# Kernel optimization log

Hardware: AMD Instinct MI355X
Metric: run time of the kernel (lower is better)

The kernel has to match this reference:

```python
import jax, jax.numpy as jnp
import numpy as np

N, C, H, W = 2, 256, 128, 128
NH, P = 8, 4
DH = C // NH
PAD = 1            # int(sqrt(n_points)//2)
HP, WP = H + 2 * PAD, W + 2 * PAD
LQ = H * W
DW_KS = 7


def _grid():
    # _generate_dilation_grids with n_points=4, dilation_rates=[1]:
    # kernel_size=2, linspace(0,1,2); torch stacks [y, x] (y-first quirk preserved)
    lin = np.linspace(0.0, 1.0, 2, dtype=np.float32)
    ky, kx = np.meshgrid(lin, lin, indexing='ij')
    return jnp.asarray(np.stack([ky, kx], -1).reshape(P, 2))  # (P, 2)


def _forward(query, reference_points, dw_kernel, dw_bias, ln_w, ln_b,
             W_off, b_off, W_attn, b_attn, W_val, b_val, W_out, b_out):
    # ---- dw_conv branch: depthwise 7x7 conv + channel LayerNorm + exact GELU ----
    q_img = query.transpose(0, 2, 1).reshape(N, C, H, W)
    q_img = jax.lax.conv_general_dilated(
        q_img, dw_kernel, (1, 1), [(3, 3), (3, 3)],
        dimension_numbers=('NCHW', 'OIHW', 'NCHW'), feature_group_count=C
    ) + dw_bias[None, :, None, None]
    mu = q_img.mean(axis=1, keepdims=True)
    var = ((q_img - mu) ** 2).mean(axis=1, keepdims=True)
    q_img = (q_img - mu) * jax.lax.rsqrt(var + 1e-5) * ln_w[None, :, None, None] + ln_b[None, :, None, None]
    q_img = jax.nn.gelu(q_img, approximate=False)
    q = q_img.transpose(0, 2, 3, 1).reshape(N, LQ, C)

    # ---- value projection + zero padding around the H x W map ----
    value = q @ W_val + b_val
    value = jnp.pad(value.reshape(N, H, W, C), ((0, 0), (PAD, PAD), (PAD, PAD), (0, 0)))
    v = value.reshape(N, HP * WP, NH, DH).transpose(0, 2, 1, 3)  # (N, NH, S, DH)

    # ---- offsets, sigmoid attention weights ----
    off = (q @ W_off + b_off).reshape(N, LQ, NH, 1, P, 2)
    attn = jax.nn.sigmoid(q @ W_attn + b_attn).reshape(N, LQ, NH, P)  # n_levels=1

    grid = _grid()[None, None, None, None, :, :]               # (1,1,1,1,P,2)
    norm = jnp.array([WP, HP], dtype=query.dtype)              # (W, H) normalizer
    loc = reference_points[:, :, None, :, None, :] + (grid + off) / norm
    loc = loc[:, :, :, 0, :, :]                                # (N, LQ, NH, P, 2)

    # grid_sample bilinear, align_corners=False, zero padding
    x = loc[..., 0] * WP - 0.5
    y = loc[..., 1] * HP - 0.5
    x0 = jnp.floor(x)
    y0 = jnp.floor(y)
    wx1 = x - x0
    wx0 = 1.0 - wx1
    wy1 = y - y0
    wy0 = 1.0 - wy1
    x0i = x0.astype(jnp.int32)
    y0i = y0.astype(jnp.int32)

    def gather(xi, yi):
        valid = (xi >= 0) & (xi < WP) & (yi >= 0) & (yi < HP)
        idx = jnp.clip(yi, 0, HP - 1) * WP + jnp.clip(xi, 0, WP - 1)
        idx = idx.transpose(0, 2, 1, 3).reshape(N, NH, LQ * P)
        g = jnp.take_along_axis(v, idx[..., None], axis=2)     # (N, NH, LQ*P, DH)
        m = valid.transpose(0, 2, 1, 3).reshape(N, NH, LQ * P, 1)
        return jnp.where(m, g, 0.0)

    def wmul(w):
        return w.transpose(0, 2, 1, 3).reshape(N, NH, LQ * P, 1)

    samp = (gather(x0i, y0i) * wmul(wx0 * wy0)
            + gather(x0i + 1, y0i) * wmul(wx1 * wy0)
            + gather(x0i, y0i + 1) * wmul(wx0 * wy1)
            + gather(x0i + 1, y0i + 1) * wmul(wx1 * wy1))      # (N, NH, LQ*P, DH)

    samp = samp.reshape(N, NH, LQ, P, DH)
    aw = attn.transpose(0, 2, 1, 3)[..., None]                 # (N, NH, LQ, P, 1)
    out = (samp * aw).sum(axis=3)                              # (N, NH, LQ, DH)
    out = out.transpose(0, 2, 1, 3).reshape(N, LQ, C)
    return out @ W_out + b_out


def setup_inputs() -> dict:
    key = jax.random.key(0)
    ks = jax.random.split(key, 8)
    return dict(
        query=jax.random.normal(ks[0], (N, LQ, C), jnp.float32),
        reference_points=jax.random.uniform(ks[1], (N, LQ, 1, 2), dtype=jnp.float32),
        input_spatial_shapes=jnp.array([[HP, WP]], dtype=jnp.int32),
        input_level_start_index=jnp.zeros((1,), dtype=jnp.int32),
        dw_kernel=jax.random.normal(ks[2], (C, 1, DW_KS, DW_KS), jnp.float32) * 0.05,
        dw_bias=jnp.zeros((C,), jnp.float32),
        ln_w=jnp.ones((C,), jnp.float32),
        ln_b=jnp.zeros((C,), jnp.float32),
        W_off=jax.random.normal(ks[3], (C, NH * P * 2), jnp.float32) * 0.01,
        b_off=jnp.zeros((NH * P * 2,), jnp.float32),
        W_attn=jax.random.normal(ks[4], (C, NH * P), jnp.float32) * 0.02,
        b_attn=jnp.zeros((NH * P,), jnp.float32),
        W_val=jax.random.normal(ks[5], (C, C), jnp.float32) * (1.0 / 16.0),
        b_val=jnp.zeros((C,), jnp.float32),
        W_out=jax.random.normal(ks[6], (C, C), jnp.float32) * (1.0 / 16.0),
        b_out=jnp.zeros((C,), jnp.float32),
    )


def reference(query, reference_points, input_spatial_shapes, input_level_start_index,
              dw_kernel, dw_bias, ln_w, ln_b, W_off, b_off, W_attn, b_attn,
              W_val, b_val, W_out, b_out):
    # input_spatial_shapes / input_level_start_index are static metadata (baked into constants)
    return _forward(query, reference_points, dw_kernel, dw_bias, ln_w, ln_b,
                    W_off, b_off, W_attn, b_attn, W_val, b_val, W_out, b_out)
```

## Files before the change

kernel.cpp:

```cpp
#include <hip/hip_runtime.h>
#include <hip/hip_bf16.h>
#include <math.h>

#define NB   2
#define CC   256
#define HH   128
#define WW   128
#define HPP  130
#define WPP  130
#define LQ   16384

typedef __attribute__((ext_vector_type(8))) short short8;
typedef __attribute__((ext_vector_type(4))) float f32x4;
typedef __attribute__((ext_vector_type(4))) unsigned int u32x4;

static __device__ __forceinline__ unsigned short f2bf(float f) {
    __hip_bfloat16 h = __float2bfloat16(f);
    return __builtin_bit_cast(unsigned short, h);
}
static __device__ __forceinline__ float bf2f(unsigned short u) {
    unsigned int x = ((unsigned int)u) << 16;
    return __builtin_bit_cast(float, x);
}

static __device__ __forceinline__ float gelu_fast(float x) {
    float u = x * x;
    float t = x * fmaf(0.044715f, u, 1.0f);
    float e = __builtin_amdgcn_exp2f(t * 2.3022083f);
    float r = __builtin_amdgcn_rcpf(e + 1.0f);
    return x - x * r;
}

__global__ __launch_bounds__(256) void prep_kernel(
    const float* __restrict__ dwk,
    const float* __restrict__ Wval,
    const float* __restrict__ Wout,
    const float* __restrict__ Woff, const float* __restrict__ boff,
    const float* __restrict__ Wattn, const float* __restrict__ battn,
    float* __restrict__ kt,
    unsigned short* __restrict__ wt_val,
    unsigned short* __restrict__ wt_out,
    unsigned short* __restrict__ wt_oa,
    float* __restrict__ b_oa)
{
    int b = blockIdx.x;
    int t = threadIdx.x;
    if (b < 49) {
        kt[b * CC + t] = dwk[t * 49 + b];
    } else if (b < 305) {
        int k = b - 49;
        wt_val[(size_t)t * 256 + k] = f2bf(Wval[(size_t)k * 256 + t]);
    } else if (b < 561) {
        int k = b - 305;
        wt_out[(size_t)t * 256 + k] = f2bf(Wout[(size_t)k * 256 + t]);
    } else {
        int k = b - 561;
        if (t < 128) {
            float v = 0.f, bb = 0.f;
            if (t < 64)      { v = Woff[(size_t)k * 64 + t];        bb = boff[t]; }
            else if (t < 96) { v = Wattn[(size_t)k * 32 + (t - 64)]; bb = battn[t - 64]; }
            wt_oa[(size_t)t * 256 + k] = f2bf(v);
            if (k == 0) b_oa[t] = bb;
        }
    }
}

__global__ __launch_bounds__(256) void zero_border_kernel(unsigned short* __restrict__ vpad)
{
    int b = blockIdx.x;
    int n = (b >= 516) ? 1 : 0;
    int i = b - n * 516;
    int y, x;
    if (i < 130)      { y = 0;           x = i; }
    else if (i < 260) { y = 129;         x = i - 130; }
    else if (i < 388) { y = i - 260 + 1; x = 0; }
    else              { y = i - 388 + 1; x = 129; }
    vpad[(((size_t)n * HPP + y) * WPP + x) * CC + threadIdx.x] = 0;
}

__global__ __launch_bounds__(256) void conv_ln_gelu_kernel(
    const float* __restrict__ q,
    const float* __restrict__ kt,
    const float* __restrict__ kbias,
    const float* __restrict__ lnw,
    const float* __restrict__ lnb,
    unsigned short* __restrict__ qact)
{
    int c  = threadIdx.x;
    int w0 = blockIdx.x * 8;
    int h  = blockIdx.y;
    int n  = blockIdx.z;

    const float* qn = q + (size_t)n * LQ * CC + c;

    float bias = kbias[c];
    float acc[8];
    #pragma unroll
    for (int i = 0; i < 8; ++i) acc[i] = bias;

    if (w0 >= 8 && w0 <= 112 && h >= 3 && h <= 124) {
        #pragma unroll
        for (int ky = 0; ky < 7; ++ky) {
            const float* qrow = qn + ((size_t)(h + ky - 3) * WW + (w0 - 3)) * CC;
            float wt[7];
            #pragma unroll
            for (int kx = 0; kx < 7; ++kx)
                wt[kx] = kt[(ky * 7 + kx) * CC + c];
            float in[14];
            #pragma unroll
            for (int j = 0; j < 14; ++j)
                in[j] = qrow[(size_t)j * CC];
            #pragma unroll
            for (int i = 0; i < 8; ++i)
                #pragma unroll
                for (int kx = 0; kx < 7; ++kx)
                    acc[i] = fmaf(in[i + kx], wt[kx], acc[i]);
        }
    } else {
        #pragma unroll
        for (int ky = 0; ky < 7; ++ky) {
            int iy = h + ky - 3;
            if (iy < 0 || iy >= HH) continue;
            float wt[7];
            #pragma unroll
            for (int kx = 0; kx < 7; ++kx)
                wt[kx] = kt[(ky * 7 + kx) * CC + c];
            float in[14];
            const float* qrow = qn + (size_t)iy * WW * CC;
            #pragma unroll
            for (int j = 0; j < 14; ++j) {
                int ix = w0 - 3 + j;
                in[j] = (ix >= 0 && ix < WW) ? qrow[(size_t)ix * CC] : 0.f;
            }
            #pragma unroll
            for (int i = 0; i < 8; ++i)
                #pragma unroll
                for (int kx = 0; kx < 7; ++kx)
                    acc[i] = fmaf(in[i + kx], wt[kx], acc[i]);
        }
    }

    __shared__ float lsum[8][4];
    __shared__ float lsq[8][4];
    int lane = threadIdx.x & 63;
    int wv   = threadIdx.x >> 6;

    #pragma unroll
    for (int i = 0; i < 8; ++i) {
        float v  = acc[i];
        float v2 = v * v;
        #pragma unroll
        for (int m = 1; m < 64; m <<= 1) {
            v  += __shfl_xor(v,  m);
            v2 += __shfl_xor(v2, m);
        }
        if (lane == 0) { lsum[i][wv] = v; lsq[i][wv] = v2; }
    }
    __syncthreads();

    float lw = lnw[c];
    float lb = lnb[c];
    unsigned short* qo = qact + (((size_t)n * LQ) + (size_t)h * WW + w0) * CC + c;

    #pragma unroll
    for (int i = 0; i < 8; ++i) {
        float s  = lsum[i][0] + lsum[i][1] + lsum[i][2] + lsum[i][3];
        float s2 = lsq[i][0]  + lsq[i][1]  + lsq[i][2]  + lsq[i][3];
        float mu  = s * (1.0f / 256.0f);
        float var = s2 * (1.0f / 256.0f) - mu * mu;
        float inv = rsqrtf(var + 1e-5f);
        float yv  = (acc[i] - mu) * inv * lw + lb;
        qo[(size_t)i * CC] = f2bf(gelu_fast(yv));
    }
}

__global__ __launch_bounds__(256) void gemm_val_oa(
    const unsigned short* __restrict__ A,
    const unsigned short* __restrict__ Bv, const float* __restrict__ bv_,
    unsigned short* __restrict__ Cv,
    const unsigned short* __restrict__ Bo, const float* __restrict__ bo_,
    float* __restrict__ Co)
{
    __shared__ unsigned short Al[128][72];
    __shared__ unsigned short Bl[128][72];

    bool oam = (blockIdx.y == 2);
    const unsigned short* Bt = oam ? Bo : Bv;
    const float* bias = oam ? bo_ : bv_;
    int bn = oam ? 0 : blockIdx.y * 128;

    int t    = threadIdx.x;
    int bm   = blockIdx.x * 128;
    int wid  = t >> 6;
    int lane = t & 63;
    int wr   = wid >> 1;
    int wc   = wid & 1;
    int lr   = lane & 15;
    int lg   = lane >> 4;

    int srow = t >> 1;
    int sseg = (t & 1) << 5;

    const unsigned short* gA = A + (size_t)(bm + srow) * 256 + sseg;
    const unsigned short* gB = Bt + (size_t)(bn + srow) * 256 + sseg;
    unsigned short* lA = &Al[srow][sseg];
    unsigned short* lB = &Bl[srow][sseg];

    f32x4 acc[4][4] = {};

    for (int kt = 0; kt < 4; ++kt) {
        const unsigned short* ga = gA + kt * 64;
        const unsigned short* gb = gB + kt * 64;
        u32x4 a0 = *(const u32x4*)(ga);
        u32x4 a1 = *(const u32x4*)(ga + 8);
        u32x4 a2 = *(const u32x4*)(ga + 16);
        u32x4 a3 = *(const u32x4*)(ga + 24);
        u32x4 b0 = *(const u32x4*)(gb);
        u32x4 b1 = *(const u32x4*)(gb + 8);
        u32x4 b2 = *(const u32x4*)(gb + 16);
        u32x4 b3 = *(const u32x4*)(gb + 24);
        *(u32x4*)(lA)      = a0;
        *(u32x4*)(lA + 8)  = a1;
        *(u32x4*)(lA + 16) = a2;
        *(u32x4*)(lA + 24) = a3;
        *(u32x4*)(lB)      = b0;
        *(u32x4*)(lB + 8)  = b1;
        *(u32x4*)(lB + 16) = b2;
        *(u32x4*)(lB + 24) = b3;
        __syncthreads();

        #pragma unroll
        for (int kk = 0; kk < 2; ++kk) {
            short8 af[4], bfr[4];
            #pragma unroll
            for (int m = 0; m < 4; ++m)
                af[m] = *(const short8*)(&Al[wr * 64 + m * 16 + lr][kk * 32 + lg * 8]);
            #pragma unroll
            for (int nn = 0; nn < 4; ++nn)
                bfr[nn] = *(const short8*)(&Bl[wc * 64 + nn * 16 + lr][kk * 32 + lg * 8]);
            #pragma unroll
            for (int m = 0; m < 4; ++m)
                #pragma unroll
                for (int nn = 0; nn < 4; ++nn)
                    acc[m][nn] = __builtin_amdgcn_mfma_f32_16x16x32_bf16(
                        af[m], bfr[nn], acc[m][nn], 0, 0, 0);
        }
        __syncthreads();
    }

    float bvv[4];
    #pragma unroll
    for (int nn = 0; nn < 4; ++nn) bvv[nn] = bias[bn + wc * 64 + nn * 16 + lr];

    #pragma unroll
    for (int m = 0; m < 4; ++m) {
        #pragma unroll
        for (int j = 0; j < 4; ++j) {
            int row = bm + wr * 64 + m * 16 + lg * 4 + j;
            if (oam) {
                size_t rbase = (size_t)row * 128;
                #pragma unroll
                for (int nn = 0; nn < 4; ++nn) {
                    int col = wc * 64 + nn * 16 + lr;
                    Co[rbase + col] = acc[m][nn][j] + bvv[nn];
                }
            } else {
                int nb = row >> 14;
                int hw = row & 16383;
                int hh = hw >> 7;
                int ww = hw & 127;
                size_t rbase = (((size_t)nb * HPP + (hh + 1)) * WPP + (ww + 1)) * CC;
                #pragma unroll
                for (int nn = 0; nn < 4; ++nn) {
                    int col = bn + wc * 64 + nn * 16 + lr;
                    Cv[rbase + col] = f2bf(acc[m][nn][j] + bvv[nn]);
                }
            }
        }
    }
}

__global__ __launch_bounds__(256) void gemm_mfma_row(
    const unsigned short* __restrict__ A,
    const unsigned short* __restrict__ Bt,
    const float* __restrict__ bias,
    float* __restrict__ C,
    int Nn)
{
    __shared__ unsigned short Al[128][72];
    __shared__ unsigned short Bl[128][72];

    int t    = threadIdx.x;
    int bm   = blockIdx.x * 128;
    int bn   = blockIdx.y * 128;
    int wid  = t >> 6;
    int lane = t & 63;
    int wr   = wid >> 1;
    int wc   = wid & 1;
    int lr   = lane & 15;
    int lg   = lane >> 4;

    int srow = t >> 1;
    int sseg = (t & 1) << 5;

    const unsigned short* gA = A + (size_t)(bm + srow) * 256 + sseg;
    const unsigned short* gB = Bt + (size_t)(bn + srow) * 256 + sseg;
    unsigned short* lA = &Al[srow][sseg];
    unsigned short* lB = &Bl[srow][sseg];

    f32x4 acc[4][4] = {};

    for (int kt = 0; kt < 4; ++kt) {
        const unsigned short* ga = gA + kt * 64;
        const unsigned short* gb = gB + kt * 64;
        u32x4 a0 = *(const u32x4*)(ga);
        u32x4 a1 = *(const u32x4*)(ga + 8);
        u32x4 a2 = *(const u32x4*)(ga + 16);
        u32x4 a3 = *(const u32x4*)(ga + 24);
        u32x4 b0 = *(const u32x4*)(gb);
        u32x4 b1 = *(const u32x4*)(gb + 8);
        u32x4 b2 = *(const u32x4*)(gb + 16);
        u32x4 b3 = *(const u32x4*)(gb + 24);
        *(u32x4*)(lA)      = a0;
        *(u32x4*)(lA + 8)  = a1;
        *(u32x4*)(lA + 16) = a2;
        *(u32x4*)(lA + 24) = a3;
        *(u32x4*)(lB)      = b0;
        *(u32x4*)(lB + 8)  = b1;
        *(u32x4*)(lB + 16) = b2;
        *(u32x4*)(lB + 24) = b3;
        __syncthreads();

        #pragma unroll
        for (int kk = 0; kk < 2; ++kk) {
            short8 af[4], bfr[4];
            #pragma unroll
            for (int m = 0; m < 4; ++m)
                af[m] = *(const short8*)(&Al[wr * 64 + m * 16 + lr][kk * 32 + lg * 8]);
            #pragma unroll
            for (int nn = 0; nn < 4; ++nn)
                bfr[nn] = *(const short8*)(&Bl[wc * 64 + nn * 16 + lr][kk * 32 + lg * 8]);
            #pragma unroll
            for (int m = 0; m < 4; ++m)
                #pragma unroll
                for (int nn = 0; nn < 4; ++nn)
                    acc[m][nn] = __builtin_amdgcn_mfma_f32_16x16x32_bf16(
                        af[m], bfr[nn], acc[m][nn], 0, 0, 0);
        }
        __syncthreads();
    }

    float bvv[4];
    #pragma unroll
    for (int nn = 0; nn < 4; ++nn) bvv[nn] = bias[bn + wc * 64 + nn * 16 + lr];

    #pragma unroll
    for (int m = 0; m < 4; ++m) {
        #pragma unroll
        for (int j = 0; j < 4; ++j) {
            int row = bm + wr * 64 + m * 16 + lg * 4 + j;
            size_t rbase = (size_t)row * Nn;
            #pragma unroll
            for (int nn = 0; nn < 4; ++nn) {
                int col = bn + wc * 64 + nn * 16 + lr;
                C[rbase + col] = acc[m][nn][j] + bvv[nn];
            }
        }
    }
}

__global__ __launch_bounds__(256) void sampler_kernel(
    const float* __restrict__ rp,
    const float* __restrict__ oa,
    const unsigned short* __restrict__ vpad,
    unsigned short* __restrict__ outb)
{
    __shared__ int4   sIdx[4][4][8];
    __shared__ float4 sW[4][4][8];

    int tid  = threadIdx.x;
    int row0 = blockIdx.x * 4;

    if (tid < 128) {
        int rl   = tid >> 5;
        int hp   = tid & 31;
        int head = hp >> 2;
        int p    = hp & 3;
        int row  = row0 + rl;

        float ref0 = rp[(size_t)row * 2 + 0];
        float ref1 = rp[(size_t)row * 2 + 1];
        float o0 = oa[(size_t)row * 128 + head * 8 + p * 2 + 0];
        float o1 = oa[(size_t)row * 128 + head * 8 + p * 2 + 1];
        float al = oa[(size_t)row * 128 + 64 + head * 4 + p];
        float a  = 1.0f / (1.0f + __builtin_amdgcn_exp2f(-al * 1.4426950409f));

        float gy = (float)(p >> 1);
        float gx = (float)(p & 1);
        float x = ref0 * WPP + gy + o0 - 0.5f;
        float y = ref1 * HPP + gx + o1 - 0.5f;

        float x0f = floorf(x), y0f = floorf(y);
        int   x0  = (int)x0f,  y0  = (int)y0f;
        float wx1 = x - x0f, wx0 = 1.f - wx1;
        float wy1 = y - y0f, wy0 = 1.f - wy1;
        int x1 = x0 + 1, y1 = y0 + 1;

        bool vx0 = (x0 >= 0) & (x0 < WPP);
        bool vx1 = (x1 >= 0) & (x1 < WPP);
        bool vy0 = (y0 >= 0) & (y0 < HPP);
        bool vy1 = (y1 >= 0) & (y1 < HPP);
        int cx0 = min(max(x0, 0), WPP - 1);
        int cx1 = min(max(x1, 0), WPP - 1);
        int cy0 = min(max(y0, 0), HPP - 1);
        int cy1 = min(max(y1, 0), HPP - 1);

        int4 id;
        id.x = cy0 * WPP + cx0;
        id.y = cy0 * WPP + cx1;
        id.z = cy1 * WPP + cx0;
        id.w = cy1 * WPP + cx1;
        float4 w;
        w.x = (vx0 && vy0) ? a * wx0 * wy0 : 0.f;
        w.y = (vx1 && vy0) ? a * wx1 * wy0 : 0.f;
        w.z = (vx0 && vy1) ? a * wx0 * wy1 : 0.f;
        w.w = (vx1 && vy1) ? a * wx1 * wy1 : 0.f;

        sIdx[rl][p][head] = id;
        sW[rl][p][head]   = w;
    }
    __syncthreads();

    int rl   = tid >> 6;
    int c0   = (tid & 63) * 4;
    int head = c0 >> 5;
    int row  = row0 + rl;
    int n    = row >> 14;
    const unsigned short* vbase = vpad + (size_t)n * HPP * WPP * CC + c0;

    float4 acc = make_float4(0.f, 0.f, 0.f, 0.f);
    #pragma unroll
    for (int p = 0; p < 4; ++p) {
        int4   id = sIdx[rl][p][head];
        float4 w  = sW[rl][p][head];
        ushort4 g0 = *reinterpret_cast<const ushort4*>(vbase + (size_t)id.x * CC);
        ushort4 g1 = *reinterpret_cast<const ushort4*>(vbase + (size_t)id.y * CC);
        ushort4 g2 = *reinterpret_cast<const ushort4*>(vbase + (size_t)id.z * CC);
        ushort4 g3 = *reinterpret_cast<const ushort4*>(vbase + (size_t)id.w * CC);
        acc.x += w.x * bf2f(g0.x) + w.y * bf2f(g1.x) + w.z * bf2f(g2.x) + w.w * bf2f(g3.x);
        acc.y += w.x * bf2f(g0.y) + w.y * bf2f(g1.y) + w.z * bf2f(g2.y) + w.w * bf2f(g3.y);
        acc.z += w.x * bf2f(g0.z) + w.y * bf2f(g1.z) + w.z * bf2f(g2.z) + w.w * bf2f(g3.z);
        acc.w += w.x * bf2f(g0.w) + w.y * bf2f(g1.w) + w.z * bf2f(g2.w) + w.w * bf2f(g3.w);
    }
    ushort4 o;
    o.x = f2bf(acc.x);
    o.y = f2bf(acc.y);
    o.z = f2bf(acc.z);
    o.w = f2bf(acc.w);
    *reinterpret_cast<ushort4*>(&outb[(size_t)row * CC + c0]) = o;
}

extern "C" void kernel_launch(void* const* d_in, const int* in_sizes, int n_in,
                              void* d_out, int out_size, void* d_ws, size_t ws_size,
                              hipStream_t stream)
{
    const float* query = (const float*)d_in[0];
    const float* rp    = (const float*)d_in[1];
    const float* dwk   = (const float*)d_in[4];
    const float* dwb   = (const float*)d_in[5];
    const float* lnw   = (const float*)d_in[6];
    const float* lnb   = (const float*)d_in[7];
    const float* Woff  = (const float*)d_in[8];
    const float* boff  = (const float*)d_in[9];
    const float* Wattn = (const float*)d_in[10];
    const float* battn = (const float*)d_in[11];
    const float* Wval  = (const float*)d_in[12];
    const float* bval  = (const float*)d_in[13];
    const float* Wout  = (const float*)d_in[14];
    const float* bout  = (const float*)d_in[15];
    float* out = (float*)d_out;

    const int M = NB * LQ;

    uint8_t* w8 = (uint8_t*)d_ws;
    unsigned short* q_act  = (unsigned short*)w8;
    unsigned short* v_pad  = (unsigned short*)(w8 + 16777216);
    float*          oa     = (float*)(w8 + 34082816);
    unsigned short* wt_val = (unsigned short*)(w8 + 50860032);
    unsigned short* wt_out = (unsigned short*)(w8 + 50991104);
    unsigned short* wt_oa  = (unsigned short*)(w8 + 51122176);
    float*          b_oa   = (float*)(w8 + 51187712);
    float*          kt     = (float*)(w8 + 51188224);
    unsigned short* out_attn = q_act;

    zero_border_kernel<<<1032, 256, 0, stream>>>(v_pad);

    prep_kernel<<<817, 256, 0, stream>>>(
        dwk, Wval, Wout, Woff, boff, Wattn, battn,
        kt, wt_val, wt_out, wt_oa, b_oa);

    {
        dim3 grid(WW / 8, HH, NB);
        conv_ln_gelu_kernel<<<grid, 256, 0, stream>>>(
            query, kt, dwb, lnw, lnb, q_act);
    }

    {
        dim3 grid(M / 128, 3);
        gemm_val_oa<<<grid, 256, 0, stream>>>(
            q_act, wt_val, bval, v_pad, wt_oa, b_oa, oa);
    }

    sampler_kernel<<<M / 4, 256, 0, stream>>>(rp, oa, v_pad, out_attn);

    {
        dim3 grid(M / 128, 2);
        gemm_mfma_row<<<grid, 256, 0, stream>>>(out_attn, wt_out, bout, out, 256);
    }
}
```

Before: 96.59 us.

## Compute two output rows per conv block and fold border zeroing into prep kernel

```diff
diff --git a/kernel.cpp b/kernel.cpp
--- a/kernel.cpp
+++ b/kernel.cpp
@@ -41,7 +41,8 @@
     unsigned short* __restrict__ wt_val,
     unsigned short* __restrict__ wt_out,
     unsigned short* __restrict__ wt_oa,
-    float* __restrict__ b_oa)
+    float* __restrict__ b_oa,
+    unsigned short* __restrict__ vpad)
 {
     int b = blockIdx.x;
     int t = threadIdx.x;
@@ -53,7 +54,7 @@
     } else if (b < 561) {
         int k = b - 305;
         wt_out[(size_t)t * 256 + k] = f2bf(Wout[(size_t)k * 256 + t]);
-    } else {
+    } else if (b < 817) {
         int k = b - 561;
         if (t < 128) {
             float v = 0.f, bb = 0.f;
@@ -62,20 +63,17 @@
             wt_oa[(size_t)t * 256 + k] = f2bf(v);
             if (k == 0) b_oa[t] = bb;
         }
-    }
-}
-
-__global__ __launch_bounds__(256) void zero_border_kernel(unsigned short* __restrict__ vpad)
-{
-    int b = blockIdx.x;
-    int n = (b >= 516) ? 1 : 0;
-    int i = b - n * 516;
-    int y, x;
-    if (i < 130)      { y = 0;           x = i; }
-    else if (i < 260) { y = 129;         x = i - 130; }
-    else if (i < 388) { y = i - 260 + 1; x = 0; }
-    else              { y = i - 388 + 1; x = 129; }
-    vpad[(((size_t)n * HPP + y) * WPP + x) * CC + threadIdx.x] = 0;
+    } else {
+        int bb = b - 817;
+        int n = (bb >= 516) ? 1 : 0;
+        int i = bb - n * 516;
+        int y, x;
+        if (i < 130)      { y = 0;           x = i; }
+        else if (i < 260) { y = 129;         x = i - 130; }
+        else if (i < 388) { y = i - 260 + 1; x = 0; }
+        else              { y = i - 388 + 1; x = 129; }
+        vpad[(((size_t)n * HPP + y) * WPP + x) * CC + t] = 0;
+    }
 }
 
 __global__ __launch_bounds__(256) void conv_ln_gelu_kernel(
@@ -88,66 +86,95 @@
 {
     int c  = threadIdx.x;
     int w0 = blockIdx.x * 8;
-    int h  = blockIdx.y;
+    int h0 = blockIdx.y * 2;
     int n  = blockIdx.z;
 
     const float* qn = q + (size_t)n * LQ * CC + c;
+    const float* ktc = kt + c;
 
     float bias = kbias[c];
-    float acc[8];
-    #pragma unroll
-    for (int i = 0; i < 8; ++i) acc[i] = bias;
-
-    if (w0 >= 8 && w0 <= 112 && h >= 3 && h <= 124) {
-        #pragma unroll
-        for (int ky = 0; ky < 7; ++ky) {
-            const float* qrow = qn + ((size_t)(h + ky - 3) * WW + (w0 - 3)) * CC;
-            float wt[7];
-            #pragma unroll
-            for (int kx = 0; kx < 7; ++kx)
-                wt[kx] = kt[(ky * 7 + kx) * CC + c];
+    float acc0[8], acc1[8];
+    #pragma unroll
+    for (int i = 0; i < 8; ++i) { acc0[i] = bias; acc1[i] = bias; }
+
+    float wt_prev[7];
+
+    if (w0 >= 8 && w0 <= 112 && h0 >= 3 && h0 <= 123) {
+        #pragma unroll
+        for (int r = 0; r < 8; ++r) {
+            const float* qrow = qn + ((size_t)(h0 - 3 + r) * WW + (w0 - 3)) * CC;
             float in[14];
             #pragma unroll
             for (int j = 0; j < 14; ++j)
                 in[j] = qrow[(size_t)j * CC];
-            #pragma unroll
-            for (int i = 0; i < 8; ++i)
+            float wt_cur[7];
+            if (r < 7) {
                 #pragma unroll
                 for (int kx = 0; kx < 7; ++kx)
-                    acc[i] = fmaf(in[i + kx], wt[kx], acc[i]);
+                    wt_cur[kx] = ktc[(r * 7 + kx) * CC];
+                #pragma unroll
+                for (int i = 0; i < 8; ++i)
+                    #pragma unroll
+                    for (int kx = 0; kx < 7; ++kx)
+                        acc0[i] = fmaf(in[i + kx], wt_cur[kx], acc0[i]);
+            }
+            if (r >= 1) {
+                #pragma unroll
+                for (int i = 0; i < 8; ++i)
+                    #pragma unroll
+                    for (int kx = 0; kx < 7; ++kx)
+                        acc1[i] = fmaf(in[i + kx], wt_prev[kx], acc1[i]);
+            }
+            if (r < 7) {
+                #pragma unroll
+                for (int kx = 0; kx < 7; ++kx) wt_prev[kx] = wt_cur[kx];
+            }
         }
     } else {
         #pragma unroll
-        for (int ky = 0; ky < 7; ++ky) {
-            int iy = h + ky - 3;
-            if (iy < 0 || iy >= HH) continue;
-            float wt[7];
-            #pragma unroll
-            for (int kx = 0; kx < 7; ++kx)
-                wt[kx] = kt[(ky * 7 + kx) * CC + c];
+        for (int r = 0; r < 8; ++r) {
+            int iy = h0 - 3 + r;
+            bool rowok = (iy >= 0 && iy < HH);
+            const float* qrow = qn + (size_t)iy * WW * CC;
             float in[14];
-            const float* qrow = qn + (size_t)iy * WW * CC;
             #pragma unroll
             for (int j = 0; j < 14; ++j) {
                 int ix = w0 - 3 + j;
-                in[j] = (ix >= 0 && ix < WW) ? qrow[(size_t)ix * CC] : 0.f;
-            }
-            #pragma unroll
-            for (int i = 0; i < 8; ++i)
+                in[j] = (rowok && ix >= 0 && ix < WW) ? qrow[(size_t)ix * CC] : 0.f;
+            }
+            float wt_cur[7];
+            if (r < 7) {
                 #pragma unroll
                 for (int kx = 0; kx < 7; ++kx)
-                    acc[i] = fmaf(in[i + kx], wt[kx], acc[i]);
-        }
-    }
-
-    __shared__ float lsum[8][4];
-    __shared__ float lsq[8][4];
+                    wt_cur[kx] = ktc[(r * 7 + kx) * CC];
+                #pragma unroll
+                for (int i = 0; i < 8; ++i)
+                    #pragma unroll
+                    for (int kx = 0; kx < 7; ++kx)
+                        acc0[i] = fmaf(in[i + kx], wt_cur[kx], acc0[i]);
+            }
+            if (r >= 1) {
+                #pragma unroll
+                for (int i = 0; i < 8; ++i)
+                    #pragma unroll
+                    for (int kx = 0; kx < 7; ++kx)
+                        acc1[i] = fmaf(in[i + kx], wt_prev[kx], acc1[i]);
+            }
+            if (r < 7) {
+                #pragma unroll
+                for (int kx = 0; kx < 7; ++kx) wt_prev[kx] = wt_cur[kx];
+            }
+        }
+    }
+
+    __shared__ float lsum[16][4];
+    __shared__ float lsq[16][4];
     int lane = threadIdx.x & 63;
     int wv   = threadIdx.x >> 6;
 
     #pragma unroll
-    for (int i = 0; i < 8; ++i) {
-        float v  = acc[i];
+    for (int i = 0; i < 16; ++i) {
+        float v  = (i < 8) ? acc0[i] : acc1[i - 8];
         float v2 = v * v;
         #pragma unroll
         for (int m = 1; m < 64; m <<= 1) {
@@ -160,17 +187,19 @@
 
     float lw = lnw[c];
     float lb = lnb[c];
-    unsigned short* qo = qact + (((size_t)n * LQ) + (size_t)h * WW + w0) * CC + c;
-
-    #pragma unroll
-    for (int i = 0; i < 8; ++i) {
+    unsigned short* qo0 = qact + (((size_t)n * LQ) + (size_t)h0 * WW + w0) * CC + c;
+
+    #pragma unroll
+    for (int i = 0; i < 16; ++i) {
         float s  = lsum[i][0] + lsum[i][1] + lsum[i][2] + lsum[i][3];
         float s2 = lsq[i][0]  + lsq[i][1]  + lsq[i][2]  + lsq[i][3];
         float mu  = s * (1.0f / 256.0f);
         float var = s2 * (1.0f / 256.0f) - mu * mu;
         float inv = rsqrtf(var + 1e-5f);
-        float yv  = (acc[i] - mu) * inv * lw + lb;
-        qo[(size_t)i * CC] = f2bf(gelu_fast(yv));
+        float a   = (i < 8) ? acc0[i] : acc1[i - 8];
+        float yv  = (a - mu) * inv * lw + lb;
+        size_t off = (i < 8) ? (size_t)i * CC : ((size_t)WW + (i - 8)) * CC;
+        qo0[off] = f2bf(gelu_fast(yv));
     }
 }
 
@@ -493,14 +522,12 @@
     float*          kt     = (float*)(w8 + 51188224);
     unsigned short* out_attn = q_act;
 
-    zero_border_kernel<<<1032, 256, 0, stream>>>(v_pad);
-
-    prep_kernel<<<817, 256, 0, stream>>>(
+    prep_kernel<<<1849, 256, 0, stream>>>(
         dwk, Wval, Wout, Woff, boff, Wattn, battn,
-        kt, wt_val, wt_out, wt_oa, b_oa);
+        kt, wt_val, wt_out, wt_oa, b_oa, v_pad);
 
     {
-        dim3 grid(WW / 8, HH, NB);
+        dim3 grid(WW / 8, HH / 2, NB);
         conv_ln_gelu_kernel<<<grid, 256, 0, stream>>>(
             query, kt, dwb, lnw, lnb, q_act);
     }
```

After: 103.3 us. +7.0%, slower.

## Convert query to fp16 and run depthwise conv with packed half2 FMAs

Applied to the files above, without the earlier changes.

```diff
diff --git a/kernel.cpp b/kernel.cpp
--- a/kernel.cpp
+++ b/kernel.cpp
@@ -1,5 +1,6 @@
 #include <hip/hip_runtime.h>
 #include <hip/hip_bf16.h>
+#include <hip/hip_fp16.h>
 #include <math.h>
 
 #define NB   2
@@ -37,23 +38,26 @@
     const float* __restrict__ Wout,
     const float* __restrict__ Woff, const float* __restrict__ boff,
     const float* __restrict__ Wattn, const float* __restrict__ battn,
-    float* __restrict__ kt,
+    const float* __restrict__ query,
+    __half* __restrict__ kth,
     unsigned short* __restrict__ wt_val,
     unsigned short* __restrict__ wt_out,
     unsigned short* __restrict__ wt_oa,
-    float* __restrict__ b_oa)
+    float* __restrict__ b_oa,
+    unsigned short* __restrict__ vpad,
+    __half* __restrict__ qh)
 {
     int b = blockIdx.x;
     int t = threadIdx.x;
     if (b < 49) {
-        kt[b * CC + t] = dwk[t * 49 + b];
+        kth[b * CC + t] = __float2half(dwk[t * 49 + b]);
     } else if (b < 305) {
         int k = b - 49;
         wt_val[(size_t)t * 256 + k] = f2bf(Wval[(size_t)k * 256 + t]);
     } else if (b < 561) {
         int k = b - 305;
         wt_out[(size_t)t * 256 + k] = f2bf(Wout[(size_t)k * 256 + t]);
-    } else {
+    } else if (b < 817) {
         int k = b - 561;
         if (t < 128) {
             float v = 0.f, bb = 0.f;
@@ -62,115 +66,141 @@
             wt_oa[(size_t)t * 256 + k] = f2bf(v);
             if (k == 0) b_oa[t] = bb;
         }
-    }
-}
-
-__global__ __launch_bounds__(256) void zero_border_kernel(unsigned short* __restrict__ vpad)
-{
-    int b = blockIdx.x;
-    int n = (b >= 516) ? 1 : 0;
-    int i = b - n * 516;
-    int y, x;
-    if (i < 130)      { y = 0;           x = i; }
-    else if (i < 260) { y = 129;         x = i - 130; }
-    else if (i < 388) { y = i - 260 + 1; x = 0; }
-    else              { y = i - 388 + 1; x = 129; }
-    vpad[(((size_t)n * HPP + y) * WPP + x) * CC + threadIdx.x] = 0;
-}
-
-__global__ __launch_bounds__(256) void conv_ln_gelu_kernel(
-    const float* __restrict__ q,
-    const float* __restrict__ kt,
+    } else if (b < 1849) {
+        int bb = b - 817;
+        int n = (bb >= 516) ? 1 : 0;
+        int i = bb - n * 516;
+        int y, x;
+        if (i < 130)      { y = 0;           x = i; }
+        else if (i < 260) { y = 129;         x = i - 130; }
+        else if (i < 388) { y = i - 260 + 1; x = 0; }
+        else              { y = i - 388 + 1; x = 129; }
+        vpad[(((size_t)n * HPP + y) * WPP + x) * CC + t] = 0;
+    } else {
+        size_t idx0 = (size_t)(b - 1849) * 2048 + (size_t)t * 8;
+        const float4* src = reinterpret_cast<const float4*>(query + idx0);
+        float4 f0 = src[0];
+        float4 f1 = src[1];
+        __half2 h0 = __floats2half2_rn(f0.x, f0.y);
+        __half2 h1 = __floats2half2_rn(f0.z, f0.w);
+        __half2 h2 = __floats2half2_rn(f1.x, f1.y);
+        __half2 h3 = __floats2half2_rn(f1.z, f1.w);
+        u32x4 o;
+        o.x = __builtin_bit_cast(unsigned int, h0);
+        o.y = __builtin_bit_cast(unsigned int, h1);
+        o.z = __builtin_bit_cast(unsigned int, h2);
+        o.w = __builtin_bit_cast(unsigned int, h3);
+        *reinterpret_cast<u32x4*>(qh + idx0) = o;
+    }
+}
+
+__global__ __launch_bounds__(128) void conv_ln_gelu_kernel(
+    const __half* __restrict__ qh,
+    const __half* __restrict__ kth,
     const float* __restrict__ kbias,
     const float* __restrict__ lnw,
     const float* __restrict__ lnb,
     unsigned short* __restrict__ qact)
 {
-    int c  = threadIdx.x;
+    int t  = threadIdx.x;
     int w0 = blockIdx.x * 8;
     int h  = blockIdx.y;
     int n  = blockIdx.z;
 
-    const float* qn = q + (size_t)n * LQ * CC + c;
-
-    float bias = kbias[c];
-    float acc[8];
-    #pragma unroll
-    for (int i = 0; i < 8; ++i) acc[i] = bias;
+    const __half2* qn  = reinterpret_cast<const __half2*>(qh + (size_t)n * LQ * CC) + t;
+    const __half2* ktc = reinterpret_cast<const __half2*>(kth) + t;
+
+    __half2 acc[8];
+    #pragma unroll
+    for (int i = 0; i < 8; ++i) acc[i] = __half2(0.f, 0.f);
 
     if (w0 >= 8 && w0 <= 112 && h >= 3 && h <= 124) {
         #pragma unroll
         for (int ky = 0; ky < 7; ++ky) {
-            const float* qrow = qn + ((size_t)(h + ky - 3) * WW + (w0 - 3)) * CC;
-            float wt[7];
+            const __half2* qrow = qn + ((size_t)(h + ky - 3) * WW + (w0 - 3)) * 128;
+            __half2 wt[7];
             #pragma unroll
             for (int kx = 0; kx < 7; ++kx)
-                wt[kx] = kt[(ky * 7 + kx) * CC + c];
-            float in[14];
+                wt[kx] = ktc[(ky * 7 + kx) * 128];
+            __half2 in[14];
             #pragma unroll
             for (int j = 0; j < 14; ++j)
-                in[j] = qrow[(size_t)j * CC];
+                in[j] = qrow[(size_t)j * 128];
             #pragma unroll
             for (int i = 0; i < 8; ++i)
                 #pragma unroll
                 for (int kx = 0; kx < 7; ++kx)
-                    acc[i] = fmaf(in[i + kx], wt[kx], acc[i]);
+                    acc[i] = __hfma2(in[i + kx], wt[kx], acc[i]);
         }
     } else {
         #pragma unroll
         for (int ky = 0; ky < 7; ++ky) {
             int iy = h + ky - 3;
             if (iy < 0 || iy >= HH) continue;
-            float wt[7];
+            const __half2* qrow = qn + (size_t)iy * WW * 128;
+            __half2 wt[7];
             #pragma unroll
             for (int kx = 0; kx < 7; ++kx)
-                wt[kx] = kt[(ky * 7 + kx) * CC + c];
-            float in[14];
-            const float* qrow = qn + (size_t)iy * WW * CC;
+                wt[kx] = ktc[(ky * 7 + kx) * 128];
+            __half2 in[14];
             #pragma unroll
             for (int j = 0; j < 14; ++j) {
                 int ix = w0 - 3 + j;
-                in[j] = (ix >= 0 && ix < WW) ? qrow[(size_t)ix * CC] : 0.f;
+                in[j] = (ix >= 0 && ix < WW) ? qrow[(size_t)ix * 128]
+                                             : __half2(0.f, 0.f);
             }
             #pragma unroll
             for (int i = 0; i < 8; ++i)
                 #pragma unroll
                 for (int kx = 0; kx < 7; ++kx)
-                    acc[i] = fmaf(in[i + kx], wt[kx], acc[i]);
-        }
-    }
-
-    __shared__ float lsum[8][4];
-    __shared__ float lsq[8][4];
-    int lane = threadIdx.x & 63;
-    int wv   = threadIdx.x >> 6;
-
+                    acc[i] = __hfma2(in[i + kx], wt[kx], acc[i]);
+        }
+    }
+
+    float b0 = kbias[2 * t];
+    float b1 = kbias[2 * t + 1];
+    float a0[8], a1[8];
     #pragma unroll
     for (int i = 0; i < 8; ++i) {
-        float v  = acc[i];
-        float v2 = v * v;
+        a0[i] = __low2float(acc[i])  + b0;
+        a1[i] = __high2float(acc[i]) + b1;
+    }
+
+    __shared__ float lsum[8][2];
+    __shared__ float lsq[8][2];
+    int lane = t & 63;
+    int wv   = t >> 6;
+
+    #pragma unroll
+    for (int i = 0; i < 8; ++i) {
+        float s  = a0[i] + a1[i];
+        float sq = a0[i] * a0[i] + a1[i] * a1[i];
         #pragma unroll
         for (int m = 1; m < 64; m <<= 1) {
-            v  += __shfl_xor(v,  m);
-            v2 += __shfl_xor(v2, m);
-        }
-        if (lane == 0) { lsum[i][wv] = v; lsq[i][wv] = v2; }
+            s  += __shfl_xor(s,  m);
+            sq += __shfl_xor(sq, m);
+        }
+        if (lane == 0) { lsum[i][wv] = s; lsq[i][wv] = sq; }
     }
     __syncthreads();
 
-    float lw = lnw[c];
-    float lb = lnb[c];
-    unsigned short* qo = qact + (((size_t)n * LQ) + (size_t)h * WW + w0) * CC + c;
+    float lw0 = lnw[2 * t], lw1 = lnw[2 * t + 1];
+    float lb0 = lnb[2 * t], lb1 = lnb[2 * t + 1];
+    unsigned short* qo = qact + (((size_t)n * LQ) + (size_t)h * WW + w0) * CC + 2 * t;
 
     #pragma unroll
     for (int i = 0; i < 8; ++i) {
-        float s  = lsum[i][0] + lsum[i][1] + lsum[i][2] + lsum[i][3];
-        float s2 = lsq[i][0]  + lsq[i][1]  + lsq[i][2]  + lsq[i][3];
+        float s   = lsum[i][0] + lsum[i][1];
+        float sq  = lsq[i][0]  + lsq[i][1];
         float mu  = s * (1.0f / 256.0f);
-        float var = s2 * (1.0f / 256.0f) - mu * mu;
+        float var = sq * (1.0f / 256.0f) - mu * mu;
         float inv = rsqrtf(var + 1e-5f);
-        float yv  = (acc[i] - mu) * inv * lw + lb;
-        qo[(size_t)i * CC] = f2bf(gelu_fast(yv));
+        float g0 = gelu_fast((a0[i] - mu) * inv * lw0 + lb0);
+        float g1 = gelu_fast((a1[i] - mu) * inv * lw1 + lb1);
+        ushort2 o;
+        o.x = f2bf(g0);
+        o.y = f2bf(g1);
+        *reinterpret_cast<ushort2*>(qo + (size_t)i * CC) = o;
     }
 }
 
@@ -486,23 +516,22 @@
     unsigned short* q_act  = (unsigned short*)w8;
     unsigned short* v_pad  = (unsigned short*)(w8 + 16777216);
     float*          oa     = (float*)(w8 + 34082816);
-    unsigned short* wt_val = (unsigned short*)(w8 + 50860032);
-    unsigned short* wt_out = (unsigned short*)(w8 + 50991104);
-    unsigned short* wt_oa  = (unsigned short*)(w8 + 51122176);
-    float*          b_oa   = (float*)(w8 + 51187712);
-    float*          kt     = (float*)(w8 + 51188224);
+    __half*         qh     = (__half*)(w8 + 50860032);
+    unsigned short* wt_val = (unsigned short*)(w8 + 67637248);
+    unsigned short* wt_out = (unsigned short*)(w8 + 67768320);
+    unsigned short* wt_oa  = (unsigned short*)(w8 + 67899392);
+    float*          b_oa   = (float*)(w8 + 67964928);
+    __half*         kth    = (__half*)(w8 + 67965440);
     unsigned short* out_attn = q_act;
 
-    zero_border_kernel<<<1032, 256, 0, stream>>>(v_pad);
-
-    prep_kernel<<<817, 256, 0, stream>>>(
-        dwk, Wval, Wout, Woff, boff, Wattn, battn,
-        kt, wt_val, wt_out, wt_oa, b_oa);
+    prep_kernel<<<5945, 256, 0, stream>>>(
+        dwk, Wval, Wout, Woff, boff, Wattn, battn, query,
+        kth, wt_val, wt_out, wt_oa, b_oa, v_pad, qh);
 
     {
         dim3 grid(WW / 8, HH, NB);
-        conv_ln_gelu_kernel<<<grid, 256, 0, stream>>>(
-            query, kt, dwb, lnw, lnb, q_act);
+        conv_ln_gelu_kernel<<<grid, 128, 0, stream>>>(
+            qh, kth, dwb, lnw, lnb, q_act);
     }
 
     {
```

Result: faster. 84.29 us (-12.7%).
